# Kernel tuning notes

Hardware: AMD Instinct MI355X
Metric: run time of the kernel (lower is better)

Reference implementation:

```python
import jax, jax.numpy as jnp
import numpy as np

N_HEADS = 8
PROJ_DIM = 32


def _phi(x):
    # elu(x) + 1 feature map (always > 0)
    return jax.nn.elu(x) + 1.0


def _causal_linear(pq, pk, v):
    # Faithful to torch _linear_kernelized_attention masked branch:
    #   dpq_l = pq_l - pq_{l-1} (with pq_{-1}=0)
    #   result_l = cumsum_{m<=l} (dpq_m . v_m) * pk_m
    # The torch code materializes (N,H,L,D,D); here the identical math is
    # computed via a per-position scalar c_m = dpq_m . v_m, O(L*D) memory.
    dpq = pq - jnp.concatenate([jnp.zeros_like(pq[..., :1, :]), pq[..., :-1, :]], axis=-2)
    c = jnp.einsum('nhld,nhld->nhl', dpq, v)[..., None]  # (N,H,L,1)
    return jnp.cumsum(c * pk, axis=-2)  # (N,H,L,D)


def _bidir_linear(pq, pk, v):
    # Non-masked linear path: (pk^T v) first, then pq @ (.)
    right = jnp.einsum('nhld,nhle->nhde', pk, v)
    return jnp.einsum('nhqd,nhde->nhqe', pq, right)


def _attention(Y, X, Wq, Wk, Wv, mask):
    N, Lq, Dm = Y.shape
    Lk = X.shape[1]
    H, Pd = N_HEADS, PROJ_DIM
    # torch Linear: x @ W^T
    q = (Y @ Wq.T).reshape(N, Lq, H, Pd).transpose(0, 2, 1, 3)  # (N,H,Lq,Pd)
    k = (X @ Wk.T).reshape(N, Lk, H, Pd).transpose(0, 2, 1, 3)
    v = (X @ Wv.T).reshape(N, Lk, H, Pd).transpose(0, 2, 1, 3)
    pq, pk = _phi(q), _phi(k)
    fn = _causal_linear if mask else _bidir_linear
    num = fn(pq, pk, v)
    den = fn(pq, pk, jnp.ones_like(v))  # v_scale = ones expanded to D
    A = num / den
    return A.transpose(0, 2, 1, 3).reshape(N, Lq, H * Pd)


def setup_inputs() -> dict:
    key = jax.random.key(0)
    kY, kX, kq, kk, kv = jax.random.split(key, 5)
    N, L, dim = 2, 8192, N_HEADS * PROJ_DIM
    scale_in = 0.05            # keep phi(q),phi(k) ~ 1 so denominator stays positive
    scale_w = 1.0 / np.sqrt(dim)
    Y = scale_in * jax.random.normal(kY, (N, L, dim), dtype=jnp.float32)
    X = scale_in * jax.random.normal(kX, (N, L, dim), dtype=jnp.float32)
    Wq = scale_w * jax.random.normal(kq, (dim, dim), dtype=jnp.float32)
    Wk = scale_w * jax.random.normal(kk, (dim, dim), dtype=jnp.float32)
    Wv = scale_w * jax.random.normal(kv, (dim, dim), dtype=jnp.float32)
    return {"Y": Y, "X": X, "Wq": Wq, "Wk": Wk, "Wv": Wv, "mask": 1}


def reference(Y, X, Wq, Wk, Wv, mask):
    return _attention(Y, X, Wq, Wk, Wv, mask)
```

## Files before the change

kernel.cpp:

```cpp
#include <hip/hip_runtime.h>
#include <hip/hip_bf16.h>


__device__ __forceinline__ float phi_f(float x) {
    return x > 0.f ? x + 1.f : __expf(x);
}

__device__ __forceinline__ unsigned short f2bf(float x) {
    __hip_bfloat16 h = __float2bfloat16(x);
    return *reinterpret_cast<unsigned short*>(&h);
}

typedef __attribute__((ext_vector_type(8))) short short8;
typedef __attribute__((ext_vector_type(4))) float f32x4;

__global__ __launch_bounds__(256) void k_qkv(
        const float* __restrict__ Y, const float* __restrict__ X,
        const float* __restrict__ Wq, const float* __restrict__ Wk,
        const float* __restrict__ Wv,
        float* __restrict__ pq, float* __restrict__ pk, float* __restrict__ v)
{
    __shared__ __align__(16) unsigned short As[64 * 40];
    __shared__ __align__(16) unsigned short Bs[256 * 40];

    const int bx  = blockIdx.x;
    const int mat = bx >> 8;
    const int rt  = bx & 255;
    const int mbase = rt * 64;
    const float* src = (mat == 0) ? Y : X;
    const float* W   = (mat == 0) ? Wq : (mat == 1 ? Wk : Wv);
    float* dst       = (mat == 0) ? pq : (mat == 1 ? pk : v);

    const int t    = threadIdx.x;
    const int lane = t & 63;
    const int nw   = (t >> 6) * 64;
    const int ln   = lane & 15;
    const int qd   = lane >> 4;

    f32x4 acc[4][4];
#pragma unroll
    for (int i = 0; i < 4; i++)
#pragma unroll
        for (int j = 0; j < 4; j++) acc[i][j] = (f32x4){0.f, 0.f, 0.f, 0.f};

    for (int kt = 0; kt < 8; kt++) {
        const int k0 = kt * 32;
#pragma unroll
        for (int i = 0; i < 2; i++) {
            const int idx = t + 256 * i;
            const int row = idx >> 3, q = idx & 7;
            float4 f = *(const float4*)(src + (size_t)(mbase + row) * 256 + k0 + q * 4);
            ushort4 h;
            h.x = f2bf(f.x); h.y = f2bf(f.y); h.z = f2bf(f.z); h.w = f2bf(f.w);
            *(ushort4*)&As[row * 40 + q * 4] = h;
        }
#pragma unroll
        for (int i = 0; i < 8; i++) {
            const int idx = t + 256 * i;
            const int row = idx >> 3, q = idx & 7;
            float4 f = *(const float4*)(W + (size_t)row * 256 + k0 + q * 4);
            ushort4 h;
            h.x = f2bf(f.x); h.y = f2bf(f.y); h.z = f2bf(f.z); h.w = f2bf(f.w);
            *(ushort4*)&Bs[row * 40 + q * 4] = h;
        }
        __syncthreads();

        short8 a[4], b[4];
#pragma unroll
        for (int i = 0; i < 4; i++)
            a[i] = *(const short8*)&As[(i * 16 + ln) * 40 + qd * 8];
#pragma unroll
        for (int j = 0; j < 4; j++)
            b[j] = *(const short8*)&Bs[(nw + j * 16 + ln) * 40 + qd * 8];
#pragma unroll
        for (int i = 0; i < 4; i++)
#pragma unroll
            for (int j = 0; j < 4; j++)
                acc[i][j] = __builtin_amdgcn_mfma_f32_16x16x32_bf16(a[i], b[j], acc[i][j], 0, 0, 0);
        __syncthreads();
    }

#pragma unroll
    for (int i = 0; i < 4; i++) {
#pragma unroll
        for (int j = 0; j < 4; j++) {
            const int col = nw + j * 16 + ln;
            const int h = col >> 5, d = col & 31;
#pragma unroll
            for (int r = 0; r < 4; r++) {
                const int rowl = i * 16 + qd * 4 + r;
                const int mg = mbase + rowl;
                const int nb = mg >> 13, l = mg & 8191;
                float val = acc[i][j][r];
                if (mat != 2) val = phi_f(val);
                dst[(((size_t)(nb * 8 + h) * 8192) + l) * 32 + d] = val;
            }
        }
    }
}

__global__ __launch_bounds__(256) void k_coef(
        const float* __restrict__ pq, const float* __restrict__ pk_,
        const float* __restrict__ v,
        float* __restrict__ c, float* __restrict__ cden,
        float* __restrict__ totals)
{
    const int b = blockIdx.x;
    const int seg = b >> 5, chunk = b & 31;
    const int t = threadIdx.x;
    const int l = chunk * 256 + t;
    const size_t base = ((size_t)seg * 8192 + l) * 32;

    __shared__ float sc[256], sd[256];
    __shared__ float spk[256 * 32];
    __shared__ float red[4][64];

    float cc = 0.f, cd = 0.f;
    {
        const float msk = (l > 0) ? 1.f : 0.f;
        const size_t pbase = (l > 0) ? base - 32 : base;
        const float4* pq4 = (const float4*)(pq + base);
        const float4* pm4 = (const float4*)(pq + pbase);
        const float4* v4  = (const float4*)(v + base);
#pragma unroll
        for (int j = 0; j < 8; j++) {
            float4 a = pq4[j];
            float4 p = pm4[j];
            float4 vv = v4[j];
            float dx = a.x - msk * p.x, dy = a.y - msk * p.y;
            float dz = a.z - msk * p.z, dw = a.w - msk * p.w;
            cc += dx * vv.x + dy * vv.y + dz * vv.z + dw * vv.w;
            cd += dx + dy + dz + dw;
        }
    }
    c[seg * 8192 + l] = cc;
    cden[seg * 8192 + l] = cd;
    sc[t] = cc;
    sd[t] = cd;

    {
        const float4* g = (const float4*)(pk_ + ((size_t)seg * 8192 + (size_t)chunk * 256) * 32);
        float4* s = (float4*)spk;
        for (int i = t; i < 2048; i += 256) s[i] = g[i];
    }
    __syncthreads();

    const int lane = t & 63, mq = t >> 6;
    const int d = lane & 31;
    const bool isden = lane >= 32;
    float tot = 0.f;
    const int m0 = mq * 64;
    for (int m = m0; m < m0 + 64; m++) {
        float coef = isden ? sd[m] : sc[m];
        tot += coef * spk[m * 32 + d];
    }
    red[mq][lane] = tot;
    __syncthreads();
    if (t < 64) {
        float s = red[0][t] + red[1][t] + red[2][t] + red[3][t];
        totals[((size_t)seg * 32 + chunk) * 64 + t] = s;
    }
}

__global__ void k_offsets(const float* __restrict__ totals, float* __restrict__ offs)
{
    const int seg = blockIdx.x;
    const int lane = threadIdx.x;
    float run = 0.f;
    for (int ch = 0; ch < 32; ch++) {
        const size_t idx = ((size_t)seg * 32 + ch) * 64 + lane;
        offs[idx] = run;
        run += totals[idx];
    }
}

__global__ __launch_bounds__(256) void k_final(
        const float* __restrict__ pk_, const float* __restrict__ c,
        const float* __restrict__ cden, const float* __restrict__ offs,
        float* __restrict__ out)
{
    const int b = blockIdx.x;
    const int seg = b >> 5, chunk = b & 31;
    const int n = seg >> 3, h = seg & 7;
    const int t = threadIdx.x;
    const int l0 = chunk * 256;

    __shared__ float spk[256 * 32];
    __shared__ float sc[256], sd[256];
    __shared__ float wsum[4][64];

    {
        const float4* g = (const float4*)(pk_ + ((size_t)seg * 8192 + l0) * 32);
        float4* s = (float4*)spk;
        for (int i = t; i < 2048; i += 256) s[i] = g[i];
    }
    sc[t] = c[seg * 8192 + l0 + t];
    sd[t] = cden[seg * 8192 + l0 + t];
    __syncthreads();

    const int lane = t & 63, wv = t >> 6;
    const int d = lane & 31;
    const bool isden = lane >= 32;
    const int m0 = wv * 64;

    float s = 0.f;
    for (int m = m0; m < m0 + 64; m++) {
        float coef = isden ? sd[m] : sc[m];
        s += coef * spk[m * 32 + d];
    }
    wsum[wv][lane] = s;
    __syncthreads();

    float run = offs[((size_t)seg * 32 + chunk) * 64 + lane];
    for (int j = 0; j < wv; j++) run += wsum[j][lane];

    size_t orow = ((size_t)n * 8192 + (size_t)(l0 + m0)) * 256 + h * 32 + d;
    for (int m = m0; m < m0 + 64; m++) {
        float coef = isden ? sd[m] : sc[m];
        run += coef * spk[m * 32 + d];
        float other = __shfl_xor(run, 32);
        if (!isden) out[orow] = run / other;
        orow += 256;
    }
}

extern "C" void kernel_launch(void* const* d_in, const int* in_sizes, int n_in,
                              void* d_out, int out_size, void* d_ws, size_t ws_size,
                              hipStream_t stream)
{
    const float* Y  = (const float*)d_in[0];
    const float* X  = (const float*)d_in[1];
    const float* Wq = (const float*)d_in[2];
    const float* Wk = (const float*)d_in[3];
    const float* Wv = (const float*)d_in[4];
    float* out = (float*)d_out;

    float* ws  = (float*)d_ws;
    float* pq  = ws;
    float* pk  = pq + 4194304;
    float* v   = pk + 4194304;
    float* c   = v  + 4194304;
    float* cd  = c  + 131072;
    float* tot = cd + 131072;
    float* off = tot + 32768;

    hipLaunchKernelGGL(k_qkv,     dim3(768), dim3(256), 0, stream, Y, X, Wq, Wk, Wv, pq, pk, v);
    hipLaunchKernelGGL(k_coef,    dim3(512), dim3(256), 0, stream, pq, pk, v, c, cd, tot);
    hipLaunchKernelGGL(k_offsets, dim3(16),  dim3(64),  0, stream, tot, off);
    hipLaunchKernelGGL(k_final,   dim3(512), dim3(256), 0, stream, pk, c, cd, off, out);
}
```

Baseline: 126.8 us.

## Fuse QKV projection with coefficient and chunk-total computation, store pk as bf16

Merges the three projection GEMMs, the per-position coefficient computation and the per-tile chunk totals into one kernel. The kernel computes q and v tile-wise and forms dpq·v in registers via shuffles, recomputing the previous row's pq to handle the tile boundary. Only phi(k) is written out, as bf16. This removes the fp32 round trips of pq, pk and v through global memory and one launch. It adds a finer 64-row offset scan and a scan kernel that stages results through shared memory for coalesced float4 output stores. The risks are only 256 blocks of 512 threads at one block per CU, serial GEMM passes per block, and bf16 rounding of pk.

```diff
diff --git a/kernel.cpp b/kernel.cpp
--- a/kernel.cpp
+++ b/kernel.cpp
@@ -2,225 +2,284 @@
 #include <hip/hip_bf16.h>
 
 
+typedef __attribute__((ext_vector_type(8))) short short8;
+typedef __attribute__((ext_vector_type(4))) float f32x4;
+
 __device__ __forceinline__ float phi_f(float x) {
     return x > 0.f ? x + 1.f : __expf(x);
 }
-
 __device__ __forceinline__ unsigned short f2bf(float x) {
     __hip_bfloat16 h = __float2bfloat16(x);
     return *reinterpret_cast<unsigned short*>(&h);
 }
-
-typedef __attribute__((ext_vector_type(8))) short short8;
-typedef __attribute__((ext_vector_type(4))) float f32x4;
-
-__global__ __launch_bounds__(256) void k_qkv(
+__device__ __forceinline__ float bf2f(unsigned short u) {
+    unsigned int v = ((unsigned int)u) << 16;
+    return __uint_as_float(v);
+}
+
+__global__ __launch_bounds__(512, 1) void k_fused(
         const float* __restrict__ Y, const float* __restrict__ X,
         const float* __restrict__ Wq, const float* __restrict__ Wk,
         const float* __restrict__ Wv,
-        float* __restrict__ pq, float* __restrict__ pk, float* __restrict__ v)
+        unsigned short* __restrict__ pk_out,
+        float* __restrict__ c_out, float* __restrict__ cd_out,
+        float* __restrict__ tot)
 {
-    __shared__ __align__(16) unsigned short As[64 * 40];
-    __shared__ __align__(16) unsigned short Bs[256 * 40];
-
-    const int bx  = blockIdx.x;
-    const int mat = bx >> 8;
-    const int rt  = bx & 255;
-    const int mbase = rt * 64;
-    const float* src = (mat == 0) ? Y : X;
-    const float* W   = (mat == 0) ? Wq : (mat == 1 ? Wk : Wv);
-    float* dst       = (mat == 0) ? pq : (mat == 1 ? pk : v);
-
-    const int t    = threadIdx.x;
+    __shared__ float scc[64][8];
+    __shared__ float scd[64][8];
+    __shared__ float spqprev[256];
+    __shared__ float yrow[256];
+    __shared__ __align__(16) unsigned short U[16896];
+    unsigned short* As = U;
+    unsigned short* Bs = U + 2560;
+    unsigned short* spkout = U;
+
+    const int bx = blockIdx.x;
+    const int mbase = bx * 64;
+    const int n = mbase >> 13;
+    const int lseg0 = mbase & 8191;
+    const int tileinseg = lseg0 >> 6;
+    const int t = threadIdx.x;
+    const int w  = t >> 6;
     const int lane = t & 63;
-    const int nw   = (t >> 6) * 64;
-    const int ln   = lane & 15;
-    const int qd   = lane >> 4;
-
-    f32x4 acc[4][4];
+    const int ln = lane & 15;
+    const int qd = lane >> 4;
+
+    auto gemm_pass = [&](const float* src, const float* W, f32x4 (&acc)[4][2]) {
+#pragma unroll
+        for (int i = 0; i < 4; i++)
+#pragma unroll
+            for (int j = 0; j < 2; j++) acc[i][j] = (f32x4){0.f, 0.f, 0.f, 0.f};
+        for (int kt = 0; kt < 8; kt++) {
+            const int k0 = kt * 32;
+            {
+                const int row = t >> 3, q = t & 7;
+                float4 f = *(const float4*)(src + (size_t)(mbase + row) * 256 + k0 + q * 4);
+                ushort4 h;
+                h.x = f2bf(f.x); h.y = f2bf(f.y); h.z = f2bf(f.z); h.w = f2bf(f.w);
+                *(ushort4*)&As[row * 40 + q * 4] = h;
+            }
+#pragma unroll
+            for (int i2 = 0; i2 < 4; i2++) {
+                const int idx = t + 512 * i2;
+                const int row = idx >> 3, q = idx & 7;
+                float4 f = *(const float4*)(W + (size_t)row * 256 + k0 + q * 4);
+                ushort4 h;
+                h.x = f2bf(f.x); h.y = f2bf(f.y); h.z = f2bf(f.z); h.w = f2bf(f.w);
+                *(ushort4*)&Bs[row * 40 + q * 4] = h;
+            }
+            __syncthreads();
+            short8 a[4], b[2];
+#pragma unroll
+            for (int i = 0; i < 4; i++)
+                a[i] = *(const short8*)&As[(i * 16 + ln) * 40 + qd * 8];
+#pragma unroll
+            for (int j = 0; j < 2; j++)
+                b[j] = *(const short8*)&Bs[(w * 32 + j * 16 + ln) * 40 + qd * 8];
+#pragma unroll
+            for (int i = 0; i < 4; i++)
+#pragma unroll
+                for (int j = 0; j < 2; j++)
+                    acc[i][j] = __builtin_amdgcn_mfma_f32_16x16x32_bf16(a[i], b[j], acc[i][j], 0, 0, 0);
+            __syncthreads();
+        }
+    };
+
+    f32x4 aq[4][2], av[4][2];
+
+    gemm_pass(Y, Wq, aq);
 #pragma unroll
     for (int i = 0; i < 4; i++)
 #pragma unroll
-        for (int j = 0; j < 4; j++) acc[i][j] = (f32x4){0.f, 0.f, 0.f, 0.f};
-
-    for (int kt = 0; kt < 8; kt++) {
-        const int k0 = kt * 32;
-#pragma unroll
-        for (int i = 0; i < 2; i++) {
-            const int idx = t + 256 * i;
-            const int row = idx >> 3, q = idx & 7;
-            float4 f = *(const float4*)(src + (size_t)(mbase + row) * 256 + k0 + q * 4);
-            ushort4 h;
-            h.x = f2bf(f.x); h.y = f2bf(f.y); h.z = f2bf(f.z); h.w = f2bf(f.w);
-            *(ushort4*)&As[row * 40 + q * 4] = h;
-        }
-#pragma unroll
-        for (int i = 0; i < 8; i++) {
-            const int idx = t + 256 * i;
-            const int row = idx >> 3, q = idx & 7;
-            float4 f = *(const float4*)(W + (size_t)row * 256 + k0 + q * 4);
-            ushort4 h;
-            h.x = f2bf(f.x); h.y = f2bf(f.y); h.z = f2bf(f.z); h.w = f2bf(f.w);
-            *(ushort4*)&Bs[row * 40 + q * 4] = h;
-        }
+        for (int j = 0; j < 2; j++)
+#pragma unroll
+            for (int r = 0; r < 4; r++) aq[i][j][r] = phi_f(aq[i][j][r]);
+
+    if (lseg0 == 0) {
+        if (t < 256) spqprev[t] = 0.f;
+    } else {
+        if (t < 64) *(float4*)&yrow[t * 4] = *(const float4*)(Y + (size_t)(mbase - 1) * 256 + t * 4);
         __syncthreads();
-
-        short8 a[4], b[4];
+        if (t < 256) {
+            const float* wr = Wq + (size_t)t * 256;
+            float s = 0.f;
+#pragma unroll 8
+            for (int k = 0; k < 256; k += 4) {
+                float4 ww = *(const float4*)(wr + k);
+                s += yrow[k] * ww.x + yrow[k + 1] * ww.y + yrow[k + 2] * ww.z + yrow[k + 3] * ww.w;
+            }
+            spqprev[t] = phi_f(s);
+        }
+    }
+    __syncthreads();
+
+    gemm_pass(X, Wv, av);
+
+    float ccr[4][4], cdr[4][4];
+#pragma unroll
+    for (int i = 0; i < 4; i++)
+#pragma unroll
+        for (int r = 0; r < 4; r++) { ccr[i][r] = 0.f; cdr[i][r] = 0.f; }
+#pragma unroll
+    for (int j = 0; j < 2; j++) {
+        float carry = spqprev[w * 32 + j * 16 + ln];
+#pragma unroll
+        for (int i = 0; i < 4; i++) {
+            const float p0 = aq[i][j][0], p1 = aq[i][j][1], p2 = aq[i][j][2], p3 = aq[i][j][3];
+            const float up3 = __shfl_up(p3, 16);
+            const float prev0 = (qd == 0) ? carry : up3;
+            const float d0 = p0 - prev0, d1 = p1 - p0, d2 = p2 - p1, d3 = p3 - p2;
+            ccr[i][0] += d0 * av[i][j][0]; cdr[i][0] += d0;
+            ccr[i][1] += d1 * av[i][j][1]; cdr[i][1] += d1;
+            ccr[i][2] += d2 * av[i][j][2]; cdr[i][2] += d2;
+            ccr[i][3] += d3 * av[i][j][3]; cdr[i][3] += d3;
+            carry = __shfl(p3, ln + 48);
+        }
+    }
+#pragma unroll
+    for (int i = 0; i < 4; i++)
+#pragma unroll
+        for (int r = 0; r < 4; r++) {
+            float x = ccr[i][r];
+            x += __shfl_xor(x, 1); x += __shfl_xor(x, 2);
+            x += __shfl_xor(x, 4); x += __shfl_xor(x, 8);
+            float y = cdr[i][r];
+            y += __shfl_xor(y, 1); y += __shfl_xor(y, 2);
+            y += __shfl_xor(y, 4); y += __shfl_xor(y, 8);
+            if (ln == 0) { scc[i * 16 + qd * 4 + r][w] = x; scd[i * 16 + qd * 4 + r][w] = y; }
+        }
+    __syncthreads();
+
+    {
+        const int hh = t >> 6, row = t & 63;
+        const size_t gi = ((size_t)(n * 8 + hh)) * 8192 + lseg0 + row;
+        c_out[gi]  = scc[row][hh];
+        cd_out[gi] = scd[row][hh];
+    }
+
+    gemm_pass(X, Wk, aq);
+#pragma unroll
+    for (int i = 0; i < 4; i++)
+#pragma unroll
+        for (int j = 0; j < 2; j++)
+#pragma unroll
+            for (int r = 0; r < 4; r++) aq[i][j][r] = phi_f(aq[i][j][r]);
+
+#pragma unroll
+    for (int j = 0; j < 2; j++) {
+        float tn = 0.f, td = 0.f;
 #pragma unroll
         for (int i = 0; i < 4; i++)
-            a[i] = *(const short8*)&As[(i * 16 + ln) * 40 + qd * 8];
-#pragma unroll
-        for (int j = 0; j < 4; j++)
-            b[j] = *(const short8*)&Bs[(nw + j * 16 + ln) * 40 + qd * 8];
+#pragma unroll
+            for (int r = 0; r < 4; r++) {
+                const int row = i * 16 + qd * 4 + r;
+                const float pv = aq[i][j][r];
+                tn += scc[row][w] * pv;
+                td += scd[row][w] * pv;
+            }
+        tn += __shfl_xor(tn, 16); tn += __shfl_xor(tn, 32);
+        td += __shfl_xor(td, 16); td += __shfl_xor(td, 32);
+        if (qd == 0) {
+            const int d = j * 16 + ln;
+            const size_t bidx = ((size_t)(n * 8 + w) * 128 + tileinseg) * 64;
+            tot[bidx + d]      = tn;
+            tot[bidx + 32 + d] = td;
+        }
+    }
+
+#pragma unroll
+    for (int j = 0; j < 2; j++)
 #pragma unroll
         for (int i = 0; i < 4; i++)
 #pragma unroll
-            for (int j = 0; j < 4; j++)
-                acc[i][j] = __builtin_amdgcn_mfma_f32_16x16x32_bf16(a[i], b[j], acc[i][j], 0, 0, 0);
-        __syncthreads();
-    }
-
-#pragma unroll
-    for (int i = 0; i < 4; i++) {
-#pragma unroll
-        for (int j = 0; j < 4; j++) {
-            const int col = nw + j * 16 + ln;
-            const int h = col >> 5, d = col & 31;
-#pragma unroll
-            for (int r = 0; r < 4; r++) {
-                const int rowl = i * 16 + qd * 4 + r;
-                const int mg = mbase + rowl;
-                const int nb = mg >> 13, l = mg & 8191;
-                float val = acc[i][j][r];
-                if (mat != 2) val = phi_f(val);
-                dst[(((size_t)(nb * 8 + h) * 8192) + l) * 32 + d] = val;
-            }
-        }
-    }
-}
-
-__global__ __launch_bounds__(256) void k_coef(
-        const float* __restrict__ pq, const float* __restrict__ pk_,
-        const float* __restrict__ v,
-        float* __restrict__ c, float* __restrict__ cden,
-        float* __restrict__ totals)
+            for (int r = 0; r < 4; r++)
+                spkout[(i * 16 + qd * 4 + r) * 264 + w * 32 + j * 16 + ln] = f2bf(aq[i][j][r]);
+    __syncthreads();
+#pragma unroll
+    for (int it = 0; it < 4; it++) {
+        const int idx = t + 512 * it;
+        const int row = idx >> 5, cg = idx & 31;
+        short8 vals = *(const short8*)&spkout[row * 264 + cg * 8];
+        const int col8 = cg * 8, hh = col8 >> 5, d8 = col8 & 31;
+        const size_t ga = (((size_t)(n * 8 + hh)) * 8192 + lseg0 + row) * 32 + d8;
+        *(short8*)(pk_out + ga) = vals;
+    }
+}
+
+__global__ __launch_bounds__(256) void k_off(
+        const float* __restrict__ tot, float* __restrict__ offs)
 {
-    const int b = blockIdx.x;
-    const int seg = b >> 5, chunk = b & 31;
-    const int t = threadIdx.x;
-    const int l = chunk * 256 + t;
-    const size_t base = ((size_t)seg * 8192 + l) * 32;
-
-    __shared__ float sc[256], sd[256];
-    __shared__ float spk[256 * 32];
-    __shared__ float red[4][64];
-
-    float cc = 0.f, cd = 0.f;
-    {
-        const float msk = (l > 0) ? 1.f : 0.f;
-        const size_t pbase = (l > 0) ? base - 32 : base;
-        const float4* pq4 = (const float4*)(pq + base);
-        const float4* pm4 = (const float4*)(pq + pbase);
-        const float4* v4  = (const float4*)(v + base);
-#pragma unroll
-        for (int j = 0; j < 8; j++) {
-            float4 a = pq4[j];
-            float4 p = pm4[j];
-            float4 vv = v4[j];
-            float dx = a.x - msk * p.x, dy = a.y - msk * p.y;
-            float dz = a.z - msk * p.z, dw = a.w - msk * p.w;
-            cc += dx * vv.x + dy * vv.y + dz * vv.z + dw * vv.w;
-            cd += dx + dy + dz + dw;
-        }
-    }
-    c[seg * 8192 + l] = cc;
-    cden[seg * 8192 + l] = cd;
-    sc[t] = cc;
-    sd[t] = cd;
-
-    {
-        const float4* g = (const float4*)(pk_ + ((size_t)seg * 8192 + (size_t)chunk * 256) * 32);
-        float4* s = (float4*)spk;
-        for (int i = t; i < 2048; i += 256) s[i] = g[i];
-    }
-    __syncthreads();
-
-    const int lane = t & 63, mq = t >> 6;
-    const int d = lane & 31;
-    const bool isden = lane >= 32;
-    float tot = 0.f;
-    const int m0 = mq * 64;
-    for (int m = m0; m < m0 + 64; m++) {
-        float coef = isden ? sd[m] : sc[m];
-        tot += coef * spk[m * 32 + d];
-    }
-    red[mq][lane] = tot;
-    __syncthreads();
-    if (t < 64) {
-        float s = red[0][t] + red[1][t] + red[2][t] + red[3][t];
-        totals[((size_t)seg * 32 + chunk) * 64 + t] = s;
-    }
-}
-
-__global__ void k_offsets(const float* __restrict__ totals, float* __restrict__ offs)
-{
-    const int seg = blockIdx.x;
-    const int lane = threadIdx.x;
+    __shared__ float wsum[4][64];
+    const int seg = blockIdx.x, t = threadIdx.x;
+    const int wv = t >> 6, lane = t & 63;
+    float s = 0.f;
+#pragma unroll
+    for (int ch = 0; ch < 32; ch++)
+        s += tot[((size_t)seg * 128 + wv * 32 + ch) * 64 + lane];
+    wsum[wv][lane] = s;
+    __syncthreads();
     float run = 0.f;
+    for (int j = 0; j < wv; j++) run += wsum[j][lane];
+#pragma unroll
     for (int ch = 0; ch < 32; ch++) {
-        const size_t idx = ((size_t)seg * 32 + ch) * 64 + lane;
+        const size_t idx = ((size_t)seg * 128 + wv * 32 + ch) * 64 + lane;
         offs[idx] = run;
-        run += totals[idx];
-    }
-}
-
-__global__ __launch_bounds__(256) void k_final(
-        const float* __restrict__ pk_, const float* __restrict__ c,
-        const float* __restrict__ cden, const float* __restrict__ offs,
+        run += tot[idx];
+    }
+}
+
+__global__ __launch_bounds__(256) void k_scan(
+        const unsigned short* __restrict__ pk, const float* __restrict__ c,
+        const float* __restrict__ cd, const float* __restrict__ offs,
         float* __restrict__ out)
 {
-    const int b = blockIdx.x;
-    const int seg = b >> 5, chunk = b & 31;
+    __shared__ float spk[256 * 32];
+    __shared__ float sc[256], sd[256];
+    __shared__ float ob[4][2][16][32];
+
+    const int bx = blockIdx.x;
+    const int seg = bx >> 5, blk = bx & 31;
     const int n = seg >> 3, h = seg & 7;
     const int t = threadIdx.x;
-    const int l0 = chunk * 256;
-
-    __shared__ float spk[256 * 32];
-    __shared__ float sc[256], sd[256];
-    __shared__ float wsum[4][64];
-
-    {
-        const float4* g = (const float4*)(pk_ + ((size_t)seg * 8192 + l0) * 32);
-        float4* s = (float4*)spk;
-        for (int i = t; i < 2048; i += 256) s[i] = g[i];
-    }
-    sc[t] = c[seg * 8192 + l0 + t];
-    sd[t] = cden[seg * 8192 + l0 + t];
-    __syncthreads();
-
-    const int lane = t & 63, wv = t >> 6;
-    const int d = lane & 31;
-    const bool isden = lane >= 32;
-    const int m0 = wv * 64;
-
-    float s = 0.f;
-    for (int m = m0; m < m0 + 64; m++) {
-        float coef = isden ? sd[m] : sc[m];
-        s += coef * spk[m * 32 + d];
-    }
-    wsum[wv][lane] = s;
-    __syncthreads();
-
-    float run = offs[((size_t)seg * 32 + chunk) * 64 + lane];
-    for (int j = 0; j < wv; j++) run += wsum[j][lane];
-
-    size_t orow = ((size_t)n * 8192 + (size_t)(l0 + m0)) * 256 + h * 32 + d;
-    for (int m = m0; m < m0 + 64; m++) {
-        float coef = isden ? sd[m] : sc[m];
-        run += coef * spk[m * 32 + d];
-        float other = __shfl_xor(run, 32);
-        if (!isden) out[orow] = run / other;
-        orow += 256;
+    const int l0 = blk * 256;
+
+#pragma unroll
+    for (int i = 0; i < 4; i++) {
+        const int idx = t + 256 * i;
+        const int row = idx >> 2, c8 = idx & 3;
+        short8 vv = *(const short8*)(pk + ((size_t)seg * 8192 + l0 + row) * 32 + c8 * 8);
+        float* dstp = &spk[row * 32 + c8 * 8];
+#pragma unroll
+        for (int e = 0; e < 8; e++) dstp[e] = bf2f((unsigned short)vv[e]);
+    }
+    sc[t] = c[(size_t)seg * 8192 + l0 + t];
+    sd[t] = cd[(size_t)seg * 8192 + l0 + t];
+    __syncthreads();
+
+    const int wv = t >> 6, lane = t & 63;
+    const int d = lane & 31, part = lane >> 5;
+    float run = offs[((size_t)seg * 128 + blk * 4 + wv) * 64 + lane];
+    const float* coefs = part ? sd : sc;
+
+    for (int mb = 0; mb < 4; mb++) {
+#pragma unroll
+        for (int p = 0; p < 16; p++) {
+            const int m = wv * 64 + mb * 16 + p;
+            run += coefs[m] * spk[m * 32 + d];
+            ob[wv][part][p][d] = run;
+        }
+        __syncthreads();
+#pragma unroll
+        for (int it = 0; it < 2; it++) {
+            const int fl = t + 256 * it;
+            const int wv2 = fl >> 7, rem = fl & 127, p = rem >> 3, d4 = rem & 7;
+            float4 nu = *(const float4*)&ob[wv2][0][p][d4 * 4];
+            float4 de = *(const float4*)&ob[wv2][1][p][d4 * 4];
+            float4 o4 = make_float4(nu.x / de.x, nu.y / de.y, nu.z / de.z, nu.w / de.w);
+            const int l = l0 + wv2 * 64 + mb * 16 + p;
+            *(float4*)(out + ((size_t)n * 8192 + l) * 256 + h * 32 + d4 * 4) = o4;
+        }
+        __syncthreads();
     }
 }
 
@@ -235,17 +294,15 @@
     const float* Wv = (const float*)d_in[4];
     float* out = (float*)d_out;
 
-    float* ws  = (float*)d_ws;
-    float* pq  = ws;
-    float* pk  = pq + 4194304;
-    float* v   = pk + 4194304;
-    float* c   = v  + 4194304;
+    float* ws = (float*)d_ws;
+    unsigned short* pk = (unsigned short*)ws;
+    float* c   = ws + 2097152;
     float* cd  = c  + 131072;
     float* tot = cd + 131072;
-    float* off = tot + 32768;
-
-    hipLaunchKernelGGL(k_qkv,     dim3(768), dim3(256), 0, stream, Y, X, Wq, Wk, Wv, pq, pk, v);
-    hipLaunchKernelGGL(k_coef,    dim3(512), dim3(256), 0, stream, pq, pk, v, c, cd, tot);
-    hipLaunchKernelGGL(k_offsets, dim3(16),  dim3(64),  0, stream, tot, off);
-    hipLaunchKernelGGL(k_final,   dim3(512), dim3(256), 0, stream, pk, c, cd, off, out);
-}
+    float* off = tot + 131072;
+
+    hipLaunchKernelGGL(k_fused, dim3(256), dim3(512), 0, stream,
+                       Y, X, Wq, Wk, Wv, pk, c, cd, tot);
+    hipLaunchKernelGGL(k_off,   dim3(16),  dim3(256), 0, stream, tot, off);
+    hipLaunchKernelGGL(k_scan,  dim3(512), dim3(256), 0, stream, pk, c, cd, off, out);
+}
```

New measurement: 138.5 us. 1.09x slower.
